# Optimization experiments

Measured on AMD Instinct MI355X. Metric: run time of the kernel, lower is better.

Reference implementation:

```python
import jax, jax.numpy as jnp
import numpy as np

B, S, DIN, DOUT = 4, 2048, 4096, 4096

def setup_inputs() -> dict:
    key = jax.random.key(0)
    k1, k2, k3, k4 = jax.random.split(key, 4)
    x = jax.random.normal(k1, (B, S, DIN), dtype=jnp.float32)
    base_T = jax.random.normal(k2, (DIN, DOUT), dtype=jnp.float32) * 0.02
    # mask bit = 1 where (finetune - base) >= 0, else 0; sign matrix = 2*mask - 1
    mask_bits = jax.random.randint(k3, (DIN, DOUT), 0, 2, dtype=jnp.int32)
    # coeff = mean |diff| quantile scalar (learned); a small positive scalar
    coeff = jax.random.uniform(k4, (1,), dtype=jnp.float32) * 0.01
    return {"x": x, "base_T": base_T, "mask_bits": mask_bits, "coeff": coeff}

def reference(x, base_T, mask_bits, coeff):
    # binary_bmm over packed mask == matmul with {-1,+1} sign matrix
    signs = (2 * mask_bits - 1).astype(x.dtype)           # [DIN, DOUT] in {-1,+1}
    dense = jnp.einsum('bsi,io->bso', x, base_T)          # x @ base.T
    corr = jnp.einsum('bsi,io->bso', x, signs)            # binary correction
    return dense + coeff[0] * corr
```

## Files before the change

kernel.cpp:

```cpp
#include <hip/hip_runtime.h>
#include <hip/hip_bf16.h>
#include <stdint.h>

#define DIN   4096
#define DOUT  4096
#define MROWS 8192

typedef __bf16 bf16_t;
typedef __attribute__((ext_vector_type(8))) __bf16 bf16x8;
typedef __attribute__((ext_vector_type(4))) float   f32x4;

__device__ __forceinline__ unsigned short f2bf(float f) {
    union { float f; unsigned u; } v; v.f = f;
    unsigned r = v.u + 0x7FFFu + ((v.u >> 16) & 1u);
    return (unsigned short)(r >> 16);
}

__global__ __launch_bounds__(256)
void build_wt(const float* __restrict__ baseT,
              const int*   __restrict__ mask,
              const float* __restrict__ coeff,
              unsigned short* __restrict__ Wt) {
    __shared__ float tile[64][68];
    const float c = coeff[0];
    const int t  = threadIdx.x;
    const int n0 = blockIdx.x * 64;
    const int k0 = blockIdx.y * 64;

    const int kr = t >> 4;
    const int nv = (t & 15) * 4;
#pragma unroll
    for (int i = 0; i < 4; ++i) {
        const int kl = i * 16 + kr;
        const size_t idx = (size_t)(k0 + kl) * DOUT + n0 + nv;
        float4 b4 = *(const float4*)(baseT + idx);
        int4   m4 = *(const int4*)(mask + idx);
        float4 v;
        v.x = b4.x + c * (float)(2 * m4.x - 1);
        v.y = b4.y + c * (float)(2 * m4.y - 1);
        v.z = b4.z + c * (float)(2 * m4.z - 1);
        v.w = b4.w + c * (float)(2 * m4.w - 1);
        *(float4*)&tile[kl][nv] = v;
    }
    __syncthreads();

    const int nr = t >> 4;
    const int kv = (t & 15) * 4;
#pragma unroll
    for (int j = 0; j < 4; ++j) {
        const int nl = j * 16 + nr;
        ushort4 o;
        o.x = f2bf(tile[kv + 0][nl]);
        o.y = f2bf(tile[kv + 1][nl]);
        o.z = f2bf(tile[kv + 2][nl]);
        o.w = f2bf(tile[kv + 3][nl]);
        *(ushort4*)(Wt + (size_t)(n0 + nl) * DIN + k0 + kv) = o;
    }
}

__global__ __launch_bounds__(256)
void cvt_x(const float* __restrict__ x, unsigned short* __restrict__ xb) {
    const int i = blockIdx.x * 256 + threadIdx.x;
    const float4* xv = (const float4*)x;
    float4 a = xv[4 * i + 0];
    float4 b = xv[4 * i + 1];
    float4 c = xv[4 * i + 2];
    float4 d = xv[4 * i + 3];
    union { ushort4 s[2]; uint4 u; } p0, p1;
    p0.s[0] = make_ushort4(f2bf(a.x), f2bf(a.y), f2bf(a.z), f2bf(a.w));
    p0.s[1] = make_ushort4(f2bf(b.x), f2bf(b.y), f2bf(b.z), f2bf(b.w));
    p1.s[0] = make_ushort4(f2bf(c.x), f2bf(c.y), f2bf(c.z), f2bf(c.w));
    p1.s[1] = make_ushort4(f2bf(d.x), f2bf(d.y), f2bf(d.z), f2bf(d.w));
    uint4* ov = (uint4*)xb;
    ov[2 * i + 0] = p0.u;
    ov[2 * i + 1] = p1.u;
}

#define AS1 __attribute__((address_space(1)))
#define AS3 __attribute__((address_space(3)))
#define GLD16(src, dst) \
    __builtin_amdgcn_global_load_lds((const AS1 void*)(src), (AS3 void*)(dst), 16, 0, 0)

#define PH_HEAD do { __builtin_amdgcn_s_barrier(); \
    asm volatile("s_waitcnt lgkmcnt(0)" ::: "memory"); \
    __builtin_amdgcn_s_setprio(1); } while (0)
#define PH_TAIL do { __builtin_amdgcn_s_setprio(0); \
    __builtin_amdgcn_s_barrier(); } while (0)
#define PH_TAIL_VM do { __builtin_amdgcn_s_setprio(0); \
    asm volatile("s_waitcnt vmcnt(4)" ::: "memory"); \
    __builtin_amdgcn_s_barrier(); } while (0)

#define STG_A(b, h, kb) do { \
    GLD16(gA + (size_t)((h) * 128 + 0) * DIN + (kb), &sA[b][(h) * 8192 + wv * 1024 + 0]);   \
    GLD16(gA + (size_t)((h) * 128 + 8) * DIN + (kb), &sA[b][(h) * 8192 + wv * 1024 + 512]); \
} while (0)
#define STG_B(b, h, kb) do { \
    GLD16(gB + (size_t)((h) * 128 + 0) * DIN + (kb), &sB[b][(h) * 8192 + wv * 1024 + 0]);   \
    GLD16(gB + (size_t)((h) * 128 + 8) * DIN + (kb), &sB[b][(h) * 8192 + wv * 1024 + 512]); \
} while (0)

#define RD_AF0(b) do { _Pragma("unroll") \
    for (int mi = 0; mi < 4; ++mi) { \
        af0[mi][0] = *(const bf16x8*)&sA[b][aRow + mi * 1024 + ko0]; \
        af0[mi][1] = *(const bf16x8*)&sA[b][aRow + mi * 1024 + ko1]; } } while (0)
#define RD_AF1(b) do { _Pragma("unroll") \
    for (int mi = 0; mi < 4; ++mi) { \
        af1[mi][0] = *(const bf16x8*)&sA[b][aRow + (4 + mi) * 1024 + ko0]; \
        af1[mi][1] = *(const bf16x8*)&sA[b][aRow + (4 + mi) * 1024 + ko1]; } } while (0)
#define RD_BF0(b) do { _Pragma("unroll") \
    for (int ni = 0; ni < 2; ++ni) { \
        bf0[ni][0] = *(const bf16x8*)&sB[b][bRow + ni * 1024 + ko0]; \
        bf0[ni][1] = *(const bf16x8*)&sB[b][bRow + ni * 1024 + ko1]; } } while (0)
#define RD_BF1(b) do { _Pragma("unroll") \
    for (int ni = 0; ni < 2; ++ni) { \
        bf1[ni][0] = *(const bf16x8*)&sB[b][bRow + (2 + ni) * 1024 + ko0]; \
        bf1[ni][1] = *(const bf16x8*)&sB[b][bRow + (2 + ni) * 1024 + ko1]; } } while (0)

#define MM(afr, mbase, bfr, nbase) do { _Pragma("unroll") \
    for (int mi = 0; mi < 4; ++mi) { _Pragma("unroll") \
        for (int ni = 0; ni < 2; ++ni) { \
            acc[(mbase) + mi][(nbase) + ni] = __builtin_amdgcn_mfma_f32_16x16x32_bf16( \
                afr[mi][0], bfr[ni][0], acc[(mbase) + mi][(nbase) + ni], 0, 0, 0); \
            acc[(mbase) + mi][(nbase) + ni] = __builtin_amdgcn_mfma_f32_16x16x32_bf16( \
                afr[mi][1], bfr[ni][1], acc[(mbase) + mi][(nbase) + ni], 0, 0, 0); } } } while (0)

__global__ __launch_bounds__(512, 2)
void gemm_bt(const unsigned short* __restrict__ X,
             const unsigned short* __restrict__ Wt,
             float* __restrict__ out) {
    __shared__ __align__(16) bf16_t sA[2][256 * 64];
    __shared__ __align__(16) bf16_t sB[2][256 * 64];

    const int tid  = threadIdx.x;
    const int lane = tid & 63;
    const int wv   = tid >> 6;
    const int wm   = wv >> 2;
    const int wn   = wv & 3;

    const int bid = blockIdx.x;
    const int wg  = (bid & 7) * 64 + (bid >> 3);
    const int bm  = wg & 31;
    const int bn  = wg >> 5;

    const int r8   = lane >> 3;
    const int kcol = ((lane & 7) ^ r8) * 8;
    const unsigned short* gA = X  + (size_t)(bm * 256 + wv * 16 + r8) * DIN + kcol;
    const unsigned short* gB = Wt + (size_t)(bn * 256 + wv * 16 + r8) * DIN + kcol;

    const int l15  = lane & 15;
    const int l7   = lane & 7;
    const int aRow = (wm * 128 + l15) * 64;
    const int bRow = (wn * 64 + l15) * 64;
    const int ko0  = (((lane >> 4) + 0) ^ l7) * 8;
    const int ko1  = (((lane >> 4) + 4) ^ l7) * 8;

    bf16x8 af0[4][2], af1[4][2], bf0[2][2], bf1[2][2];
    f32x4 acc[8][4];
#pragma unroll
    for (int i = 0; i < 8; ++i)
#pragma unroll
        for (int j = 0; j < 4; ++j) acc[i][j] = (f32x4){0.f, 0.f, 0.f, 0.f};

    STG_A(0, 0, 0); STG_A(0, 1, 0);
    STG_B(0, 0, 0); STG_B(0, 1, 0);
    STG_A(1, 0, 64); STG_A(1, 1, 64);
    asm volatile("s_waitcnt vmcnt(4)" ::: "memory");
    __builtin_amdgcn_s_barrier();

#pragma unroll 1
    for (int it = 0; it < DIN / 128; ++it) {
        const int kB1 = it * 128 + 64;
        const int k0  = (it * 128 + 128) & (DIN - 1);
        const int kA1 = (it * 128 + 192) & (DIN - 1);

        RD_AF0(0); RD_BF0(0); STG_B(1, 0, kB1);
        asm volatile("s_waitcnt lgkmcnt(8)" ::: "memory");
        PH_HEAD; MM(af0, 0, bf0, 0); PH_TAIL;
        RD_AF1(0); STG_B(1, 1, kB1);
        PH_HEAD; MM(af1, 4, bf0, 0); PH_TAIL;
        RD_BF1(0); STG_A(0, 0, k0);
        PH_HEAD; MM(af1, 4, bf1, 2); PH_TAIL;
        STG_A(0, 1, k0);
        PH_HEAD; MM(af0, 0, bf1, 2); PH_TAIL_VM;

        RD_AF0(1); RD_BF0(1); STG_B(0, 0, k0);
        asm volatile("s_waitcnt lgkmcnt(8)" ::: "memory");
        PH_HEAD; MM(af0, 0, bf0, 0); PH_TAIL;
        RD_AF1(1); STG_B(0, 1, k0);
        PH_HEAD; MM(af1, 4, bf0, 0); PH_TAIL;
        RD_BF1(1); STG_A(1, 0, kA1);
        PH_HEAD; MM(af1, 4, bf1, 2); PH_TAIL;
        STG_A(1, 1, kA1);
        PH_HEAD; MM(af0, 0, bf1, 2); PH_TAIL_VM;
    }

    const int crow0 = bm * 256 + wm * 128 + (lane >> 4) * 4;
    const int ccol0 = bn * 256 + wn * 64 + l15;
#pragma unroll
    for (int mi = 0; mi < 8; ++mi)
#pragma unroll
        for (int ni = 0; ni < 4; ++ni)
#pragma unroll
            for (int r = 0; r < 4; ++r)
                out[(size_t)(crow0 + mi * 16 + r) * DOUT + (ccol0 + ni * 16)] =
                    acc[mi][ni][r];
}

extern "C" void kernel_launch(void* const* d_in, const int* in_sizes, int n_in,
                              void* d_out, int out_size, void* d_ws, size_t ws_size,
                              hipStream_t stream) {
    const float* x     = (const float*)d_in[0];
    const float* baseT = (const float*)d_in[1];
    const int*   mask  = (const int*)d_in[2];
    const float* coeff = (const float*)d_in[3];

    unsigned short* Wt = (unsigned short*)d_ws;
    unsigned short* Xb = (unsigned short*)((char*)d_ws + (size_t)DIN * DOUT * 2);
    float* out = (float*)d_out;

    build_wt<<<dim3(DOUT / 64, DIN / 64), 256, 0, stream>>>(baseT, mask, coeff, Wt);

    cvt_x<<<(MROWS * DIN / 16) / 256, 256, 0, stream>>>(x, Xb);

    gemm_bt<<<(MROWS / 256) * (DOUT / 256), 512, 0, stream>>>(Xb, Wt, out);
}
```

Measured before the change: 600.0 us.

## Merge prep kernels into one launch and restructure GEMM B-tile prefetch schedule

Fuses the weight-build and x-conversion kernels into a single launch, with blocks split by index, to remove one launch and its tail gap. In the GEMM main loop, B tiles are now issued together with A tiles one full stage ahead, the prologue preloads both A and B for stage 1, and the vmcnt wait is raised to match. This gives loads more time in flight but increases outstanding loads and changes the ordering between stores into a buffer and reads from it.

```diff
diff --git a/kernel.cpp b/kernel.cpp
--- a/kernel.cpp
+++ b/kernel.cpp
@@ -17,63 +17,66 @@
 }
 
 __global__ __launch_bounds__(256)
-void build_wt(const float* __restrict__ baseT,
-              const int*   __restrict__ mask,
-              const float* __restrict__ coeff,
-              unsigned short* __restrict__ Wt) {
+void prep(const float* __restrict__ x,
+          const float* __restrict__ baseT,
+          const int*   __restrict__ mask,
+          const float* __restrict__ coeff,
+          unsigned short* __restrict__ Wt,
+          unsigned short* __restrict__ xb) {
     __shared__ float tile[64][68];
-    const float c = coeff[0];
-    const int t  = threadIdx.x;
-    const int n0 = blockIdx.x * 64;
-    const int k0 = blockIdx.y * 64;
-
-    const int kr = t >> 4;
-    const int nv = (t & 15) * 4;
-#pragma unroll
-    for (int i = 0; i < 4; ++i) {
-        const int kl = i * 16 + kr;
-        const size_t idx = (size_t)(k0 + kl) * DOUT + n0 + nv;
-        float4 b4 = *(const float4*)(baseT + idx);
-        int4   m4 = *(const int4*)(mask + idx);
-        float4 v;
-        v.x = b4.x + c * (float)(2 * m4.x - 1);
-        v.y = b4.y + c * (float)(2 * m4.y - 1);
-        v.z = b4.z + c * (float)(2 * m4.z - 1);
-        v.w = b4.w + c * (float)(2 * m4.w - 1);
-        *(float4*)&tile[kl][nv] = v;
+    const int b = blockIdx.x;
+    const int t = threadIdx.x;
+
+    if (b < 4096) {
+        const float c = coeff[0];
+        const int n0 = (b & 63) * 64;
+        const int k0 = (b >> 6) * 64;
+
+        const int kr = t >> 4;
+        const int nv = (t & 15) * 4;
+#pragma unroll
+        for (int i = 0; i < 4; ++i) {
+            const int kl = i * 16 + kr;
+            const size_t idx = (size_t)(k0 + kl) * DOUT + n0 + nv;
+            float4 b4 = *(const float4*)(baseT + idx);
+            int4   m4 = *(const int4*)(mask + idx);
+            float4 v;
+            v.x = b4.x + c * (float)(2 * m4.x - 1);
+            v.y = b4.y + c * (float)(2 * m4.y - 1);
+            v.z = b4.z + c * (float)(2 * m4.z - 1);
+            v.w = b4.w + c * (float)(2 * m4.w - 1);
+            *(float4*)&tile[kl][nv] = v;
+        }
+        __syncthreads();
+
+        const int nr = t >> 4;
+        const int kv = (t & 15) * 4;
+#pragma unroll
+        for (int j = 0; j < 4; ++j) {
+            const int nl = j * 16 + nr;
+            ushort4 o;
+            o.x = f2bf(tile[kv + 0][nl]);
+            o.y = f2bf(tile[kv + 1][nl]);
+            o.z = f2bf(tile[kv + 2][nl]);
+            o.w = f2bf(tile[kv + 3][nl]);
+            *(ushort4*)(Wt + (size_t)(n0 + nl) * DIN + k0 + kv) = o;
+        }
+    } else {
+        const int i = (b - 4096) * 256 + t;
+        const float4* xv = (const float4*)x;
+        float4 a = xv[4 * i + 0];
+        float4 bb = xv[4 * i + 1];
+        float4 cc = xv[4 * i + 2];
+        float4 d = xv[4 * i + 3];
+        union { ushort4 s[2]; uint4 u; } p0, p1;
+        p0.s[0] = make_ushort4(f2bf(a.x), f2bf(a.y), f2bf(a.z), f2bf(a.w));
+        p0.s[1] = make_ushort4(f2bf(bb.x), f2bf(bb.y), f2bf(bb.z), f2bf(bb.w));
+        p1.s[0] = make_ushort4(f2bf(cc.x), f2bf(cc.y), f2bf(cc.z), f2bf(cc.w));
+        p1.s[1] = make_ushort4(f2bf(d.x), f2bf(d.y), f2bf(d.z), f2bf(d.w));
+        uint4* ov = (uint4*)xb;
+        ov[2 * i + 0] = p0.u;
+        ov[2 * i + 1] = p1.u;
     }
-    __syncthreads();
-
-    const int nr = t >> 4;
-    const int kv = (t & 15) * 4;
-#pragma unroll
-    for (int j = 0; j < 4; ++j) {
-        const int nl = j * 16 + nr;
-        ushort4 o;
-        o.x = f2bf(tile[kv + 0][nl]);
-        o.y = f2bf(tile[kv + 1][nl]);
-        o.z = f2bf(tile[kv + 2][nl]);
-        o.w = f2bf(tile[kv + 3][nl]);
-        *(ushort4*)(Wt + (size_t)(n0 + nl) * DIN + k0 + kv) = o;
-    }
-}
-
-__global__ __launch_bounds__(256)
-void cvt_x(const float* __restrict__ x, unsigned short* __restrict__ xb) {
-    const int i = blockIdx.x * 256 + threadIdx.x;
-    const float4* xv = (const float4*)x;
-    float4 a = xv[4 * i + 0];
-    float4 b = xv[4 * i + 1];
-    float4 c = xv[4 * i + 2];
-    float4 d = xv[4 * i + 3];
-    union { ushort4 s[2]; uint4 u; } p0, p1;
-    p0.s[0] = make_ushort4(f2bf(a.x), f2bf(a.y), f2bf(a.z), f2bf(a.w));
-    p0.s[1] = make_ushort4(f2bf(b.x), f2bf(b.y), f2bf(b.z), f2bf(b.w));
-    p1.s[0] = make_ushort4(f2bf(c.x), f2bf(c.y), f2bf(c.z), f2bf(c.w));
-    p1.s[1] = make_ushort4(f2bf(d.x), f2bf(d.y), f2bf(d.z), f2bf(d.w));
-    uint4* ov = (uint4*)xb;
-    ov[2 * i + 0] = p0.u;
-    ov[2 * i + 1] = p1.u;
 }
 
 #define AS1 __attribute__((address_space(1)))
@@ -87,7 +90,7 @@
 #define PH_TAIL do { __builtin_amdgcn_s_setprio(0); \
     __builtin_amdgcn_s_barrier(); } while (0)
 #define PH_TAIL_VM do { __builtin_amdgcn_s_setprio(0); \
-    asm volatile("s_waitcnt vmcnt(4)" ::: "memory"); \
+    asm volatile("s_waitcnt vmcnt(8)" ::: "memory"); \
     __builtin_amdgcn_s_barrier(); } while (0)
 
 #define STG_A(b, h, kb) do { \
@@ -161,36 +164,36 @@
 #pragma unroll
         for (int j = 0; j < 4; ++j) acc[i][j] = (f32x4){0.f, 0.f, 0.f, 0.f};
 
-    STG_A(0, 0, 0); STG_A(0, 1, 0);
-    STG_B(0, 0, 0); STG_B(0, 1, 0);
+    STG_A(0, 0, 0);  STG_A(0, 1, 0);
+    STG_B(0, 0, 0);  STG_B(0, 1, 0);
     STG_A(1, 0, 64); STG_A(1, 1, 64);
-    asm volatile("s_waitcnt vmcnt(4)" ::: "memory");
+    STG_B(1, 0, 64); STG_B(1, 1, 64);
+    asm volatile("s_waitcnt vmcnt(8)" ::: "memory");
     __builtin_amdgcn_s_barrier();
 
 #pragma unroll 1
     for (int it = 0; it < DIN / 128; ++it) {
-        const int kB1 = it * 128 + 64;
         const int k0  = (it * 128 + 128) & (DIN - 1);
         const int kA1 = (it * 128 + 192) & (DIN - 1);
 
-        RD_AF0(0); RD_BF0(0); STG_B(1, 0, kB1);
+        RD_AF0(0); RD_BF0(0);
         asm volatile("s_waitcnt lgkmcnt(8)" ::: "memory");
         PH_HEAD; MM(af0, 0, bf0, 0); PH_TAIL;
-        RD_AF1(0); STG_B(1, 1, kB1);
+        RD_AF1(0);
         PH_HEAD; MM(af1, 4, bf0, 0); PH_TAIL;
         RD_BF1(0); STG_A(0, 0, k0);
         PH_HEAD; MM(af1, 4, bf1, 2); PH_TAIL;
-        STG_A(0, 1, k0);
+        STG_A(0, 1, k0); STG_B(0, 0, k0); STG_B(0, 1, k0);
         PH_HEAD; MM(af0, 0, bf1, 2); PH_TAIL_VM;
 
-        RD_AF0(1); RD_BF0(1); STG_B(0, 0, k0);
+        RD_AF0(1); RD_BF0(1);
         asm volatile("s_waitcnt lgkmcnt(8)" ::: "memory");
         PH_HEAD; MM(af0, 0, bf0, 0); PH_TAIL;
-        RD_AF1(1); STG_B(0, 1, k0);
+        RD_AF1(1);
         PH_HEAD; MM(af1, 4, bf0, 0); PH_TAIL;
         RD_BF1(1); STG_A(1, 0, kA1);
         PH_HEAD; MM(af1, 4, bf1, 2); PH_TAIL;
-        STG_A(1, 1, kA1);
+        STG_A(1, 1, kA1); STG_B(1, 0, kA1); STG_B(1, 1, kA1);
         PH_HEAD; MM(af0, 0, bf1, 2); PH_TAIL_VM;
     }
 
@@ -218,9 +221,7 @@
     unsigned short* Xb = (unsigned short*)((char*)d_ws + (size_t)DIN * DOUT * 2);
     float* out = (float*)d_out;
 
-    build_wt<<<dim3(DOUT / 64, DIN / 64), 256, 0, stream>>>(baseT, mask, coeff, Wt);
-
-    cvt_x<<<(MROWS * DIN / 16) / 256, 256, 0, stream>>>(x, Xb);
+    prep<<<4096 + (MROWS * DIN / 16) / 256, 256, 0, stream>>>(x, baseT, mask, coeff, Wt, Xb);
 
     gemm_bt<<<(MROWS / 256) * (DOUT / 256), 512, 0, stream>>>(Xb, Wt, out);
 }
```

After: 586.0 us. 2.3% less time.
